# Optimization experiments

Measured on AMD Instinct MI355X. Metric: run time of the kernel, lower is better.

Reference implementation:

```python
import jax, jax.numpy as jnp
import numpy as np

B, S, D = 4, 2048, 1024
DFF = 4 * D
NE = 4        # routed experts
NS = 2        # shared experts
TOPK = 2
CAP_F = 1.25


def _gelu(v):
    return jax.nn.gelu(v, approximate=False)  # torch nn.GELU default (erf)


def setup_inputs() -> dict:
    key = jax.random.key(0)
    ks = jax.random.split(key, 9)
    s = 0.02
    f = lambda k, sh: jax.random.normal(k, sh, dtype=jnp.float32) * s
    return {
        "hidden_states": jax.random.normal(ks[0], (B, S, D), dtype=jnp.float32),
        "router_w1": f(ks[1], (D, D)), "router_b1": jnp.zeros((D,), jnp.float32),
        "router_w2": f(ks[2], (D, NE)), "router_b2": jnp.zeros((NE,), jnp.float32),
        "re_w1": f(ks[3], (NE, D, DFF)), "re_b1": jnp.zeros((NE, DFF), jnp.float32),
        "re_w2": f(ks[4], (NE, DFF, D)), "re_b2": jnp.zeros((NE, D), jnp.float32),
        "se_w1": f(ks[5], (NS, D, DFF)), "se_b1": jnp.zeros((NS, DFF), jnp.float32),
        "se_w2": f(ks[6], (NS, DFF, D)), "se_b2": jnp.zeros((NS, D), jnp.float32),
        "out_w": f(ks[7], (D, D)), "out_b": jnp.zeros((D,), jnp.float32),
    }


def reference(hidden_states, router_w1, router_b1, router_w2, router_b2,
              re_w1, re_b1, re_w2, re_b2, se_w1, se_b1, se_w2, se_b2,
              out_w, out_b):
    b, s, d = hidden_states.shape
    T = b * s
    x = hidden_states.reshape(T, d)

    # --- router ---
    logits = _gelu(x @ router_w1 + router_b1) @ router_w2 + router_b2  # [T, NE]
    top_v, top_i = jax.lax.top_k(logits, TOPK)
    rweights = jax.nn.softmax(top_v, axis=-1)                          # [T, TOPK]
    z_loss = jnp.mean(jnp.square(jax.nn.logsumexp(logits, axis=-1)))

    capacity = int(T / NE * CAP_F)  # static Python int

    # padded token slot T absorbs dropped/overflow contributions, discarded later
    x_pad = jnp.concatenate([x, jnp.zeros((1, d), x.dtype)], axis=0)
    final = jnp.zeros((T + 1, d), x.dtype)

    for i in range(TOPK):
        eidx = top_i[:, i]
        w_pad = jnp.concatenate([rweights[:, i], jnp.zeros((1,), x.dtype)])
        for j in range(NE):
            # first `capacity` tokens routed to expert j (deterministic capacity drop)
            idx = jnp.nonzero(eidx == j, size=capacity, fill_value=T)[0]  # [capacity]
            h = _gelu(x_pad[idx] @ re_w1[j] + re_b1[j]) @ re_w2[j] + re_b2[j]
            final = final.at[idx].add(w_pad[idx][:, None] * h)
    final = final[:T]

    # shared experts (dense, weight 1/NS each)
    for j in range(NS):
        final = final + (1.0 / NS) * (_gelu(x @ se_w1[j] + se_b1[j]) @ se_w2[j] + se_b2[j])

    out = final @ out_w + out_b
    out = out * 0.5 + x * 0.5
    mu = jnp.mean(out, axis=-1, keepdims=True)
    var = jnp.var(out, axis=-1, keepdims=True)
    out = (out - mu) / jnp.sqrt(var + 1e-6)  # layer_norm, no affine, eps=1e-6
    return out.reshape(b, s, d), z_loss
```

## Files before the change

kernel.cpp:

```cpp
#include <hip/hip_runtime.h>
#include <hip/hip_bf16.h>
#include <math.h>

#define TTOK 8192
#define DM 1024
#define DFFN 4096
#define NEXP 4
#define CAPACITY 2560
#define EROWSN (2*CAPACITY)

typedef short bf16x8 __attribute__((ext_vector_type(8)));
typedef float f32x4 __attribute__((ext_vector_type(4)));

__device__ __forceinline__ unsigned short f2bf(float f) {
  unsigned int u = __float_as_uint(f);
  u = (u + 0x7fffu + ((u >> 16) & 1u)) >> 16;
  return (unsigned short)u;
}
__device__ __forceinline__ float bf2f(unsigned short h) {
  return __uint_as_float(((unsigned int)h) << 16);
}
__device__ __forceinline__ float gelu_f(float v) {
  return 0.5f * v * (1.0f + erff(v * 0.7071067811865476f));
}
__device__ __forceinline__ void gl16(const void* g, void* l) {
  __builtin_amdgcn_global_load_lds((const __attribute__((address_space(1))) void*)g,
                                   (__attribute__((address_space(3))) void*)l, 16, 0, 0);
}

__global__ void k_cvt_x(const float* __restrict__ x, unsigned short* __restrict__ xhi,
                        unsigned short* __restrict__ xlo) {
  int i = blockIdx.x * blockDim.x + threadIdx.x;
  const int n4 = (TTOK + 1) * DM / 4;
  if (i >= n4) return;
  int base = i * 4;
  float v[4] = {0.f, 0.f, 0.f, 0.f};
  if (base < TTOK * DM) {
    float4 f = *reinterpret_cast<const float4*>(x + base);
    v[0] = f.x; v[1] = f.y; v[2] = f.z; v[3] = f.w;
  }
  ushort4 h, l;
  unsigned short hh[4], ll[4];
#pragma unroll
  for (int j = 0; j < 4; j++) {
    hh[j] = f2bf(v[j]);
    ll[j] = f2bf(v[j] - bf2f(hh[j]));
  }
  h.x = hh[0]; h.y = hh[1]; h.z = hh[2]; h.w = hh[3];
  l.x = ll[0]; l.y = ll[1]; l.z = ll[2]; l.w = ll[3];
  reinterpret_cast<ushort4*>(xhi)[i] = h;
  reinterpret_cast<ushort4*>(xlo)[i] = l;
}

__global__ void k_tcvt(const float* __restrict__ W, unsigned short* __restrict__ Wt,
                       int K, int N) {
  __shared__ float tile[32][33];
  int tx = threadIdx.x, ty = threadIdx.y;
  int n0 = blockIdx.x * 32, k0 = blockIdx.y * 32;
#pragma unroll
  for (int i = 0; i < 4; i++)
    tile[ty + i * 8][tx] = W[(size_t)(k0 + ty + i * 8) * N + n0 + tx];
  __syncthreads();
#pragma unroll
  for (int i = 0; i < 4; i++)
    Wt[(size_t)(n0 + ty + i * 8) * K + k0 + tx] = f2bf(tile[tx][ty + i * 8]);
}

__global__ void k_tcvt2(const float* __restrict__ W, unsigned short* __restrict__ Whi,
                        unsigned short* __restrict__ Wlo, int K, int N) {
  __shared__ float tile[32][33];
  int tx = threadIdx.x, ty = threadIdx.y;
  int n0 = blockIdx.x * 32, k0 = blockIdx.y * 32;
#pragma unroll
  for (int i = 0; i < 4; i++)
    tile[ty + i * 8][tx] = W[(size_t)(k0 + ty + i * 8) * N + n0 + tx];
  __syncthreads();
#pragma unroll
  for (int i = 0; i < 4; i++) {
    float v = tile[tx][ty + i * 8];
    unsigned short h = f2bf(v);
    Whi[(size_t)(n0 + ty + i * 8) * K + k0 + tx] = h;
    Wlo[(size_t)(n0 + ty + i * 8) * K + k0 + tx] = f2bf(v - bf2f(h));
  }
}

__global__ __launch_bounds__(256) void k_router(
    const unsigned short* __restrict__ xhi, const unsigned short* __restrict__ xlo,
    const unsigned short* __restrict__ whi, const unsigned short* __restrict__ wlo,
    const float* __restrict__ bias, float* __restrict__ Hr) {
  const int t = threadIdx.x;
  const int m0 = blockIdx.y * 128, n0 = blockIdx.x * 128;
  __shared__ unsigned short sAh[4096], sAl[4096], sBh[4096], sBl[4096];
  const int offA0 = t * 16, offA1 = offA0 + 4096;
  const int r0 = offA0 >> 6, c0e = (offA0 & 63) >> 1;
  const int r1 = offA1 >> 6, c1e = (offA1 & 63) >> 1;
  const unsigned short* pAh0 = xhi + (size_t)(m0 + r0) * DM + c0e;
  const unsigned short* pAh1 = xhi + (size_t)(m0 + r1) * DM + c1e;
  const unsigned short* pAl0 = xlo + (size_t)(m0 + r0) * DM + c0e;
  const unsigned short* pAl1 = xlo + (size_t)(m0 + r1) * DM + c1e;
  const unsigned short* pBh0 = whi + (size_t)(n0 + r0) * DM + c0e;
  const unsigned short* pBh1 = whi + (size_t)(n0 + r1) * DM + c1e;
  const unsigned short* pBl0 = wlo + (size_t)(n0 + r0) * DM + c0e;
  const unsigned short* pBl1 = wlo + (size_t)(n0 + r1) * DM + c1e;
  const int lane = t & 63, wid = t >> 6;
  const int wm = (wid >> 1) * 64, wn = (wid & 1) * 64;
  const int fr = lane & 15, fk = (lane >> 4) * 8;
  f32x4 acc[4][4];
#pragma unroll
  for (int m = 0; m < 4; m++)
#pragma unroll
    for (int n = 0; n < 4; n++) acc[m][n] = (f32x4){0.f, 0.f, 0.f, 0.f};
  for (int k0 = 0; k0 < DM; k0 += 32) {
    __syncthreads();
    gl16(pAh0 + k0, sAh + (offA0 >> 1)); gl16(pAh1 + k0, sAh + (offA1 >> 1));
    gl16(pAl0 + k0, sAl + (offA0 >> 1)); gl16(pAl1 + k0, sAl + (offA1 >> 1));
    gl16(pBh0 + k0, sBh + (offA0 >> 1)); gl16(pBh1 + k0, sBh + (offA1 >> 1));
    gl16(pBl0 + k0, sBl + (offA0 >> 1)); gl16(pBl1 + k0, sBl + (offA1 >> 1));
    __syncthreads();
    bf16x8 ah[4], al[4], bh[4], bl[4];
#pragma unroll
    for (int m = 0; m < 4; m++) {
      ah[m] = *reinterpret_cast<const bf16x8*>(sAh + (wm + m * 16 + fr) * 32 + fk);
      al[m] = *reinterpret_cast<const bf16x8*>(sAl + (wm + m * 16 + fr) * 32 + fk);
    }
#pragma unroll
    for (int n = 0; n < 4; n++) {
      bh[n] = *reinterpret_cast<const bf16x8*>(sBh + (wn + n * 16 + fr) * 32 + fk);
      bl[n] = *reinterpret_cast<const bf16x8*>(sBl + (wn + n * 16 + fr) * 32 + fk);
    }
#pragma unroll
    for (int m = 0; m < 4; m++)
#pragma unroll
      for (int n = 0; n < 4; n++) {
        acc[m][n] = __builtin_amdgcn_mfma_f32_16x16x32_bf16(ah[m], bh[n], acc[m][n], 0, 0, 0);
        acc[m][n] = __builtin_amdgcn_mfma_f32_16x16x32_bf16(ah[m], bl[n], acc[m][n], 0, 0, 0);
        acc[m][n] = __builtin_amdgcn_mfma_f32_16x16x32_bf16(al[m], bh[n], acc[m][n], 0, 0, 0);
      }
  }
  const int er = (lane >> 4) * 4, ec = lane & 15;
#pragma unroll
  for (int n = 0; n < 4; n++) {
    const int cc = n0 + wn + n * 16 + ec;
    const float bn = bias[cc];
#pragma unroll
    for (int m = 0; m < 4; m++) {
      const int rbase = m0 + wm + m * 16 + er;
#pragma unroll
      for (int j = 0; j < 4; j++)
        Hr[(size_t)(rbase + j) * DM + cc] = gelu_f(acc[m][n][j] + bn);
    }
  }
}

template <int MODE>
__global__ __launch_bounds__(256) void k_gemm(
    const unsigned short* __restrict__ A, const unsigned short* __restrict__ Bt,
    const float* __restrict__ bias, float* __restrict__ outF,
    unsigned short* __restrict__ outBf, const int* __restrict__ rows,
    const float* __restrict__ rwgt, const int* __restrict__ rowsPad, int N, int K) {
  if constexpr (MODE == 0 || MODE == 2) {
    if ((int)(blockIdx.y * 128) >= rowsPad[0]) return;
  }
  const int t = threadIdx.x;
  const int m0 = blockIdx.y * 128, n0 = blockIdx.x * 128;
  __shared__ unsigned short sA[4096], sB[4096];
  const int offA0 = t * 16, offA1 = offA0 + 4096;
  const int r0 = offA0 >> 6, c0e = (offA0 & 63) >> 1;
  const int r1 = offA1 >> 6, c1e = (offA1 & 63) >> 1;
  size_t ar0 = m0 + r0, ar1 = m0 + r1;
  if constexpr (MODE == 0) { ar0 = rows[ar0]; ar1 = rows[ar1]; }
  const unsigned short* pA0 = A + ar0 * (size_t)K + c0e;
  const unsigned short* pA1 = A + ar1 * (size_t)K + c1e;
  const unsigned short* pB0 = Bt + (size_t)(n0 + r0) * K + c0e;
  const unsigned short* pB1 = Bt + (size_t)(n0 + r1) * K + c1e;
  unsigned short* lA0 = sA + (offA0 >> 1);
  unsigned short* lA1 = sA + (offA1 >> 1);
  unsigned short* lB0 = sB + (offA0 >> 1);
  unsigned short* lB1 = sB + (offA1 >> 1);
  const int lane = t & 63, wid = t >> 6;
  const int wm = (wid >> 1) * 64, wn = (wid & 1) * 64;
  const int fr = lane & 15, fk = (lane >> 4) * 8;
  f32x4 acc[4][4];
#pragma unroll
  for (int m = 0; m < 4; m++)
#pragma unroll
    for (int n = 0; n < 4; n++) acc[m][n] = (f32x4){0.f, 0.f, 0.f, 0.f};
  for (int k0 = 0; k0 < K; k0 += 32) {
    __syncthreads();
    gl16(pA0 + k0, lA0); gl16(pA1 + k0, lA1);
    gl16(pB0 + k0, lB0); gl16(pB1 + k0, lB1);
    __syncthreads();
    bf16x8 av[4], bv[4];
#pragma unroll
    for (int m = 0; m < 4; m++)
      av[m] = *reinterpret_cast<const bf16x8*>(sA + (wm + m * 16 + fr) * 32 + fk);
#pragma unroll
    for (int n = 0; n < 4; n++)
      bv[n] = *reinterpret_cast<const bf16x8*>(sB + (wn + n * 16 + fr) * 32 + fk);
#pragma unroll
    for (int m = 0; m < 4; m++)
#pragma unroll
      for (int n = 0; n < 4; n++)
        acc[m][n] = __builtin_amdgcn_mfma_f32_16x16x32_bf16(av[m], bv[n], acc[m][n], 0, 0, 0);
  }
  const int er = (lane >> 4) * 4, ec = lane & 15;
#pragma unroll
  for (int n = 0; n < 4; n++) {
    const int cc = n0 + wn + n * 16 + ec;
    const float bn = bias[cc];
#pragma unroll
    for (int m = 0; m < 4; m++) {
      const int rbase = m0 + wm + m * 16 + er;
#pragma unroll
      for (int j = 0; j < 4; j++) {
        const int rr = rbase + j;
        float v = acc[m][n][j] + bn;
        if constexpr (MODE <= 1) {
          outBf[(size_t)rr * N + cc] = f2bf(gelu_f(v));
        } else if constexpr (MODE == 2) {
          const int tok = rows[rr];
          if (tok < TTOK) atomicAdd(outF + (size_t)tok * DM + cc, rwgt[rr] * v);
        } else if constexpr (MODE == 3) {
          atomicAdd(outF + (size_t)rr * DM + cc, 0.5f * v);
        } else {
          outF[(size_t)rr * N + cc] = v;
        }
      }
    }
  }
}

__global__ __launch_bounds__(256) void k_logits(const float* __restrict__ Hr,
                                                const float* __restrict__ w2,
                                                const float* __restrict__ b2,
                                                float* __restrict__ logits) {
  int tok = blockIdx.x * 4 + (threadIdx.x >> 6);
  int lane = threadIdx.x & 63;
  const float* h = Hr + (size_t)tok * DM;
  float s0 = 0.f, s1 = 0.f, s2 = 0.f, s3 = 0.f;
  for (int d = lane; d < DM; d += 64) {
    float hv = h[d];
    s0 += hv * w2[d * 4 + 0];
    s1 += hv * w2[d * 4 + 1];
    s2 += hv * w2[d * 4 + 2];
    s3 += hv * w2[d * 4 + 3];
  }
#pragma unroll
  for (int off = 32; off >= 1; off >>= 1) {
    s0 += __shfl_down(s0, off, 64);
    s1 += __shfl_down(s1, off, 64);
    s2 += __shfl_down(s2, off, 64);
    s3 += __shfl_down(s3, off, 64);
  }
  if (lane == 0) {
    logits[tok * 4 + 0] = s0 + b2[0];
    logits[tok * 4 + 1] = s1 + b2[1];
    logits[tok * 4 + 2] = s2 + b2[2];
    logits[tok * 4 + 3] = s3 + b2[3];
  }
}

__global__ void k_topk(const float* __restrict__ logits, int* __restrict__ e0,
                       int* __restrict__ e1, float* __restrict__ w0,
                       float* __restrict__ w1, float* __restrict__ zout) {
  int tok = blockIdx.x * blockDim.x + threadIdx.x;
  if (tok >= TTOK) return;
  float l[4];
#pragma unroll
  for (int j = 0; j < 4; j++) l[j] = logits[tok * 4 + j];
  int i0 = 0; float v0 = l[0];
#pragma unroll
  for (int j = 1; j < 4; j++) if (l[j] > v0) { v0 = l[j]; i0 = j; }
  int i1 = -1; float v1 = -1e30f;
#pragma unroll
  for (int j = 0; j < 4; j++) if (j != i0 && l[j] > v1) { v1 = l[j]; i1 = j; }
  float d = expf(v1 - v0);
  float a = 1.f / (1.f + d);
  e0[tok] = i0; e1[tok] = i1;
  w0[tok] = a;  w1[tok] = d * a;
  float se = 0.f;
#pragma unroll
  for (int j = 0; j < 4; j++) se += expf(l[j] - v0);
  float lse = v0 + logf(se);
  atomicAdd(zout, lse * lse * (1.0f / TTOK));
}

__global__ __launch_bounds__(256) void k_lists(const int* __restrict__ e0,
                                               const int* __restrict__ e1,
                                               const float* __restrict__ w0,
                                               const float* __restrict__ w1,
                                               int* __restrict__ list,
                                               float* __restrict__ lwgt,
                                               int* __restrict__ cnt) {
  int b = blockIdx.x;
  int prio = b >> 2, j = b & 3;
  const int* e = prio ? e1 : e0;
  const float* w = prio ? w1 : w0;
  __shared__ int warpsum[4];
  __shared__ int sbase;
  if (threadIdx.x == 0) sbase = 0;
  __syncthreads();
  int lane = threadIdx.x & 63, wv = threadIdx.x >> 6;
  for (int t0 = 0; t0 < TTOK; t0 += 256) {
    int tok = t0 + threadIdx.x;
    bool p = (e[tok] == j);
    unsigned long long bal = __ballot(p);
    int pre = __popcll(bal & ((1ull << lane) - 1ull));
    if (lane == 0) warpsum[wv] = __popcll(bal);
    __syncthreads();
    int woff = 0;
    for (int q = 0; q < wv; q++) woff += warpsum[q];
    int tot = warpsum[0] + warpsum[1] + warpsum[2] + warpsum[3];
    int slot = sbase + woff + pre;
    if (p && slot < CAPACITY) {
      list[b * CAPACITY + slot] = tok;
      lwgt[b * CAPACITY + slot] = w[tok];
    }
    __syncthreads();
    if (threadIdx.x == 0) sbase += tot;
  }
  __syncthreads();
  if (threadIdx.x == 0) cnt[b] = min(sbase, CAPACITY);
}

__global__ void k_combine(const int* __restrict__ list, const float* __restrict__ lwgt,
                          const int* __restrict__ cnt, int* __restrict__ erows,
                          float* __restrict__ ewgt, int* __restrict__ rowsPad) {
  int j = blockIdx.x;
  int c0 = cnt[j], c1 = cnt[4 + j];
  for (int s = threadIdx.x; s < EROWSN; s += blockDim.x) {
    int tok = TTOK; float wv = 0.f;
    if (s < c0) { tok = list[j * CAPACITY + s]; wv = lwgt[j * CAPACITY + s]; }
    else if (s < c0 + c1) {
      tok = list[(4 + j) * CAPACITY + (s - c0)];
      wv = lwgt[(4 + j) * CAPACITY + (s - c0)];
    }
    erows[j * EROWSN + s] = tok;
    ewgt[j * EROWSN + s] = wv;
  }
  if (threadIdx.x == 0) rowsPad[j] = ((c0 + c1 + 127) / 128) * 128;
}

__global__ void k_cvt_final(const float* __restrict__ f, unsigned short* __restrict__ fb) {
  int i = blockIdx.x * blockDim.x + threadIdx.x;
  if (i >= TTOK * DM / 4) return;
  float4 v = reinterpret_cast<const float4*>(f)[i];
  ushort4 o;
  o.x = f2bf(v.x); o.y = f2bf(v.y); o.z = f2bf(v.z); o.w = f2bf(v.w);
  reinterpret_cast<ushort4*>(fb)[i] = o;
}

__global__ __launch_bounds__(256) void k_ln(const float* __restrict__ OUT,
                                            const float* __restrict__ x,
                                            float* __restrict__ out) {
  int r = blockIdx.x;
  const float* o = OUT + (size_t)r * DM;
  const float* xr = x + (size_t)r * DM;
  int t = threadIdx.x;
  float v[4];
  float s = 0.f, s2 = 0.f;
#pragma unroll
  for (int i = 0; i < 4; i++) {
    int d = t + i * 256;
    float val = 0.5f * o[d] + 0.5f * xr[d];
    v[i] = val; s += val; s2 += val * val;
  }
#pragma unroll
  for (int off = 32; off >= 1; off >>= 1) {
    s += __shfl_down(s, off, 64);
    s2 += __shfl_down(s2, off, 64);
  }
  __shared__ float rs[4], rs2[4];
  int wv = t >> 6, lane = t & 63;
  if (lane == 0) { rs[wv] = s; rs2[wv] = s2; }
  __syncthreads();
  s = rs[0] + rs[1] + rs[2] + rs[3];
  s2 = rs2[0] + rs2[1] + rs2[2] + rs2[3];
  float mu = s * (1.f / DM);
  float var = s2 * (1.f / DM) - mu * mu;
  float inv = 1.0f / sqrtf(var + 1e-6f);
#pragma unroll
  for (int i = 0; i < 4; i++)
    out[(size_t)r * DM + t + i * 256] = (v[i] - mu) * inv;
}

static constexpr size_t SZ_X = (size_t)(TTOK + 1) * DM * 2;
static constexpr size_t OFF_XHI = 0;
static constexpr size_t OFF_XLO = OFF_XHI + SZ_X;
static constexpr size_t OFF_FINAL = OFF_XLO + SZ_X;
static constexpr size_t OFF_BIG = OFF_FINAL + (size_t)TTOK * DM * 4;
static constexpr size_t OFF_WBUF = OFF_BIG + (size_t)TTOK * DFFN * 2;
static constexpr size_t OFF_MISC = OFF_WBUF + (size_t)2 * DM * DFFN * 2;
static constexpr size_t OFF_LOGITS = OFF_MISC;
static constexpr size_t OFF_E0 = OFF_LOGITS + (size_t)TTOK * 4 * 4;
static constexpr size_t OFF_E1 = OFF_E0 + (size_t)TTOK * 4;
static constexpr size_t OFF_W0 = OFF_E1 + (size_t)TTOK * 4;
static constexpr size_t OFF_W1 = OFF_W0 + (size_t)TTOK * 4;
static constexpr size_t OFF_LIST = OFF_W1 + (size_t)TTOK * 4;
static constexpr size_t OFF_LWGT = OFF_LIST + (size_t)8 * CAPACITY * 4;
static constexpr size_t OFF_CNT = OFF_LWGT + (size_t)8 * CAPACITY * 4;
static constexpr size_t OFF_EROWS = OFF_CNT + 64;
static constexpr size_t OFF_EWGT = OFF_EROWS + (size_t)NEXP * EROWSN * 4;
static constexpr size_t OFF_RPAD = OFF_EWGT + (size_t)NEXP * EROWSN * 4;

extern "C" void kernel_launch(void* const* d_in, const int* in_sizes, int n_in,
                              void* d_out, int out_size, void* d_ws, size_t ws_size,
                              hipStream_t stream) {
  const float* x = (const float*)d_in[0];
  const float* rw1 = (const float*)d_in[1];
  const float* rb1 = (const float*)d_in[2];
  const float* rw2 = (const float*)d_in[3];
  const float* rb2 = (const float*)d_in[4];
  const float* re_w1 = (const float*)d_in[5];
  const float* re_b1 = (const float*)d_in[6];
  const float* re_w2 = (const float*)d_in[7];
  const float* re_b2 = (const float*)d_in[8];
  const float* se_w1 = (const float*)d_in[9];
  const float* se_b1 = (const float*)d_in[10];
  const float* se_w2 = (const float*)d_in[11];
  const float* se_b2 = (const float*)d_in[12];
  const float* out_w = (const float*)d_in[13];
  const float* out_b = (const float*)d_in[14];
  float* outp = (float*)d_out;

  char* ws = (char*)d_ws;
  unsigned short* xhi = (unsigned short*)(ws + OFF_XHI);
  unsigned short* xlo = (unsigned short*)(ws + OFF_XLO);
  float* finalb = (float*)(ws + OFF_FINAL);
  char* big = ws + OFF_BIG;
  float* Hr = (float*)big;
  unsigned short* act = (unsigned short*)big;
  unsigned short* fbf = (unsigned short*)big;
  float* OUTb = (float*)(big + (size_t)TTOK * DM * 2);
  unsigned short* w1t = (unsigned short*)(ws + OFF_WBUF);
  unsigned short* w2t = w1t + (size_t)DM * DFFN;
  unsigned short* rwhi = w1t;
  unsigned short* rwlo = w1t + (size_t)DM * DM;
  unsigned short* owt = w1t;
  float* logits = (float*)(ws + OFF_LOGITS);
  int* e0 = (int*)(ws + OFF_E0);
  int* e1 = (int*)(ws + OFF_E1);
  float* w0 = (float*)(ws + OFF_W0);
  float* w1 = (float*)(ws + OFF_W1);
  int* list = (int*)(ws + OFF_LIST);
  float* lwgt = (float*)(ws + OFF_LWGT);
  int* cnt = (int*)(ws + OFF_CNT);
  int* erows = (int*)(ws + OFF_EROWS);
  float* ewgt = (float*)(ws + OFF_EWGT);
  int* rpad = (int*)(ws + OFF_RPAD);
  float* zout = outp + (size_t)TTOK * DM;

  hipMemsetAsync(finalb, 0, (size_t)TTOK * DM * 4, stream);
  hipMemsetAsync(zout, 0, 4, stream);

  {
    int n4 = (TTOK + 1) * DM / 4;
    k_cvt_x<<<(n4 + 255) / 256, 256, 0, stream>>>(x, xhi, xlo);
  }
  k_tcvt2<<<dim3(DM / 32, DM / 32), dim3(32, 8), 0, stream>>>(rw1, rwhi, rwlo, DM, DM);
  k_router<<<dim3(DM / 128, TTOK / 128), 256, 0, stream>>>(xhi, xlo, rwhi, rwlo, rb1, Hr);
  k_logits<<<TTOK / 4, 256, 0, stream>>>(Hr, rw2, rb2, logits);
  k_topk<<<TTOK / 256, 256, 0, stream>>>(logits, e0, e1, w0, w1, zout);
  k_lists<<<8, 256, 0, stream>>>(e0, e1, w0, w1, list, lwgt, cnt);
  k_combine<<<NEXP, 256, 0, stream>>>(list, lwgt, cnt, erows, ewgt, rpad);

  for (int j = 0; j < NEXP; j++) {
    k_tcvt<<<dim3(DFFN / 32, DM / 32), dim3(32, 8), 0, stream>>>(
        re_w1 + (size_t)j * DM * DFFN, w1t, DM, DFFN);
    k_tcvt<<<dim3(DM / 32, DFFN / 32), dim3(32, 8), 0, stream>>>(
        re_w2 + (size_t)j * DFFN * DM, w2t, DFFN, DM);
    k_gemm<0><<<dim3(DFFN / 128, EROWSN / 128), 256, 0, stream>>>(
        xhi, w1t, re_b1 + (size_t)j * DFFN, nullptr, act,
        erows + (size_t)j * EROWSN, nullptr, rpad + j, DFFN, DM);
    k_gemm<2><<<dim3(DM / 128, EROWSN / 128), 256, 0, stream>>>(
        act, w2t, re_b2 + (size_t)j * DM, finalb, nullptr,
        erows + (size_t)j * EROWSN, ewgt + (size_t)j * EROWSN, rpad + j, DM, DFFN);
  }
  for (int j = 0; j < 2; j++) {
    k_tcvt<<<dim3(DFFN / 32, DM / 32), dim3(32, 8), 0, stream>>>(
        se_w1 + (size_t)j * DM * DFFN, w1t, DM, DFFN);
    k_tcvt<<<dim3(DM / 32, DFFN / 32), dim3(32, 8), 0, stream>>>(
        se_w2 + (size_t)j * DFFN * DM, w2t, DFFN, DM);
    k_gemm<1><<<dim3(DFFN / 128, TTOK / 128), 256, 0, stream>>>(
        xhi, w1t, se_b1 + (size_t)j * DFFN, nullptr, act, nullptr, nullptr, nullptr,
        DFFN, DM);
    k_gemm<3><<<dim3(DM / 128, TTOK / 128), 256, 0, stream>>>(
        act, w2t, se_b2 + (size_t)j * DM, finalb, nullptr, nullptr, nullptr, nullptr,
        DM, DFFN);
  }
  k_cvt_final<<<TTOK * DM / 4 / 256, 256, 0, stream>>>(finalb, fbf);
  k_tcvt<<<dim3(DM / 32, DM / 32), dim3(32, 8), 0, stream>>>(out_w, owt, DM, DM);
  k_gemm<4><<<dim3(DM / 128, TTOK / 128), 256, 0, stream>>>(
      fbf, owt, out_b, OUTb, nullptr, nullptr, nullptr, nullptr, DM, DM);
  k_ln<<<TTOK, 256, 0, stream>>>(OUTb, x, outp);
}
```

Before: 1.461 ms.

## Double-buffer LDS in GEMMs, split-K expert down-proj, drop shared-expert atomics

Both the router GEMM and the generic GEMM now double-buffer their LDS tiles, so the next K slice is issued before computing on the current one, with one barrier per iteration instead of two. The expert down-projection (MODE 2) is split along K into two z-blocks to raise occupancy, with the bias added only by the first half. The shared-expert accumulation replaces atomicAdd with a plain read-modify-write, since no two blocks write the same output element there. The workspace layout is also reshuffled so xlo shares the activation buffer, and a barrier in k_lists is moved inside its loop. The doubled LDS use may lower occupancy, and split-K doubles the atomic traffic in the expert down-projection.

```diff
diff --git a/kernel.cpp b/kernel.cpp
--- a/kernel.cpp
+++ b/kernel.cpp
@@ -90,8 +90,9 @@
     const float* __restrict__ bias, float* __restrict__ Hr) {
   const int t = threadIdx.x;
   const int m0 = blockIdx.y * 128, n0 = blockIdx.x * 128;
-  __shared__ unsigned short sAh[4096], sAl[4096], sBh[4096], sBl[4096];
+  __shared__ unsigned short sAh[2][4096], sAl[2][4096], sBh[2][4096], sBl[2][4096];
   const int offA0 = t * 16, offA1 = offA0 + 4096;
+  const int i0 = offA0 >> 1, i1 = offA1 >> 1;
   const int r0 = offA0 >> 6, c0e = (offA0 & 63) >> 1;
   const int r1 = offA1 >> 6, c1e = (offA1 & 63) >> 1;
   const unsigned short* pAh0 = xhi + (size_t)(m0 + r0) * DM + c0e;
@@ -110,23 +111,29 @@
   for (int m = 0; m < 4; m++)
 #pragma unroll
     for (int n = 0; n < 4; n++) acc[m][n] = (f32x4){0.f, 0.f, 0.f, 0.f};
+
+  auto stage = [&](int b, int k) {
+    gl16(pAh0 + k, &sAh[b][i0]); gl16(pAh1 + k, &sAh[b][i1]);
+    gl16(pAl0 + k, &sAl[b][i0]); gl16(pAl1 + k, &sAl[b][i1]);
+    gl16(pBh0 + k, &sBh[b][i0]); gl16(pBh1 + k, &sBh[b][i1]);
+    gl16(pBl0 + k, &sBl[b][i0]); gl16(pBl1 + k, &sBl[b][i1]);
+  };
+
+  int cur = 0;
+  stage(0, 0);
+  __syncthreads();
   for (int k0 = 0; k0 < DM; k0 += 32) {
-    __syncthreads();
-    gl16(pAh0 + k0, sAh + (offA0 >> 1)); gl16(pAh1 + k0, sAh + (offA1 >> 1));
-    gl16(pAl0 + k0, sAl + (offA0 >> 1)); gl16(pAl1 + k0, sAl + (offA1 >> 1));
-    gl16(pBh0 + k0, sBh + (offA0 >> 1)); gl16(pBh1 + k0, sBh + (offA1 >> 1));
-    gl16(pBl0 + k0, sBl + (offA0 >> 1)); gl16(pBl1 + k0, sBl + (offA1 >> 1));
-    __syncthreads();
+    if (k0 + 32 < DM) stage(cur ^ 1, k0 + 32);
     bf16x8 ah[4], al[4], bh[4], bl[4];
 #pragma unroll
     for (int m = 0; m < 4; m++) {
-      ah[m] = *reinterpret_cast<const bf16x8*>(sAh + (wm + m * 16 + fr) * 32 + fk);
-      al[m] = *reinterpret_cast<const bf16x8*>(sAl + (wm + m * 16 + fr) * 32 + fk);
+      ah[m] = *reinterpret_cast<const bf16x8*>(&sAh[cur][(wm + m * 16 + fr) * 32 + fk]);
+      al[m] = *reinterpret_cast<const bf16x8*>(&sAl[cur][(wm + m * 16 + fr) * 32 + fk]);
     }
 #pragma unroll
     for (int n = 0; n < 4; n++) {
-      bh[n] = *reinterpret_cast<const bf16x8*>(sBh + (wn + n * 16 + fr) * 32 + fk);
-      bl[n] = *reinterpret_cast<const bf16x8*>(sBl + (wn + n * 16 + fr) * 32 + fk);
+      bh[n] = *reinterpret_cast<const bf16x8*>(&sBh[cur][(wn + n * 16 + fr) * 32 + fk]);
+      bl[n] = *reinterpret_cast<const bf16x8*>(&sBl[cur][(wn + n * 16 + fr) * 32 + fk]);
     }
 #pragma unroll
     for (int m = 0; m < 4; m++)
@@ -136,6 +143,8 @@
         acc[m][n] = __builtin_amdgcn_mfma_f32_16x16x32_bf16(ah[m], bl[n], acc[m][n], 0, 0, 0);
         acc[m][n] = __builtin_amdgcn_mfma_f32_16x16x32_bf16(al[m], bh[n], acc[m][n], 0, 0, 0);
       }
+    __syncthreads();
+    cur ^= 1;
   }
   const int er = (lane >> 4) * 4, ec = lane & 15;
 #pragma unroll
@@ -163,20 +172,19 @@
   }
   const int t = threadIdx.x;
   const int m0 = blockIdx.y * 128, n0 = blockIdx.x * 128;
-  __shared__ unsigned short sA[4096], sB[4096];
+  int kbeg = 0, klen = K;
+  if constexpr (MODE == 2) { kbeg = blockIdx.z * (K >> 1); klen = K >> 1; }
+  __shared__ unsigned short sA[2][4096], sB[2][4096];
   const int offA0 = t * 16, offA1 = offA0 + 4096;
+  const int i0 = offA0 >> 1, i1 = offA1 >> 1;
   const int r0 = offA0 >> 6, c0e = (offA0 & 63) >> 1;
   const int r1 = offA1 >> 6, c1e = (offA1 & 63) >> 1;
   size_t ar0 = m0 + r0, ar1 = m0 + r1;
   if constexpr (MODE == 0) { ar0 = rows[ar0]; ar1 = rows[ar1]; }
-  const unsigned short* pA0 = A + ar0 * (size_t)K + c0e;
-  const unsigned short* pA1 = A + ar1 * (size_t)K + c1e;
-  const unsigned short* pB0 = Bt + (size_t)(n0 + r0) * K + c0e;
-  const unsigned short* pB1 = Bt + (size_t)(n0 + r1) * K + c1e;
-  unsigned short* lA0 = sA + (offA0 >> 1);
-  unsigned short* lA1 = sA + (offA1 >> 1);
-  unsigned short* lB0 = sB + (offA0 >> 1);
-  unsigned short* lB1 = sB + (offA1 >> 1);
+  const unsigned short* pA0 = A + ar0 * (size_t)K + kbeg + c0e;
+  const unsigned short* pA1 = A + ar1 * (size_t)K + kbeg + c1e;
+  const unsigned short* pB0 = Bt + (size_t)(n0 + r0) * K + kbeg + c0e;
+  const unsigned short* pB1 = Bt + (size_t)(n0 + r1) * K + kbeg + c1e;
   const int lane = t & 63, wid = t >> 6;
   const int wm = (wid >> 1) * 64, wn = (wid & 1) * 64;
   const int fr = lane & 15, fk = (lane >> 4) * 8;
@@ -185,23 +193,31 @@
   for (int m = 0; m < 4; m++)
 #pragma unroll
     for (int n = 0; n < 4; n++) acc[m][n] = (f32x4){0.f, 0.f, 0.f, 0.f};
-  for (int k0 = 0; k0 < K; k0 += 32) {
-    __syncthreads();
-    gl16(pA0 + k0, lA0); gl16(pA1 + k0, lA1);
-    gl16(pB0 + k0, lB0); gl16(pB1 + k0, lB1);
-    __syncthreads();
+
+  auto stage = [&](int b, int k) {
+    gl16(pA0 + k, &sA[b][i0]); gl16(pA1 + k, &sA[b][i1]);
+    gl16(pB0 + k, &sB[b][i0]); gl16(pB1 + k, &sB[b][i1]);
+  };
+
+  int cur = 0;
+  stage(0, 0);
+  __syncthreads();
+  for (int k0 = 0; k0 < klen; k0 += 32) {
+    if (k0 + 32 < klen) stage(cur ^ 1, k0 + 32);
     bf16x8 av[4], bv[4];
 #pragma unroll
     for (int m = 0; m < 4; m++)
-      av[m] = *reinterpret_cast<const bf16x8*>(sA + (wm + m * 16 + fr) * 32 + fk);
+      av[m] = *reinterpret_cast<const bf16x8*>(&sA[cur][(wm + m * 16 + fr) * 32 + fk]);
 #pragma unroll
     for (int n = 0; n < 4; n++)
-      bv[n] = *reinterpret_cast<const bf16x8*>(sB + (wn + n * 16 + fr) * 32 + fk);
+      bv[n] = *reinterpret_cast<const bf16x8*>(&sB[cur][(wn + n * 16 + fr) * 32 + fk]);
 #pragma unroll
     for (int m = 0; m < 4; m++)
 #pragma unroll
       for (int n = 0; n < 4; n++)
         acc[m][n] = __builtin_amdgcn_mfma_f32_16x16x32_bf16(av[m], bv[n], acc[m][n], 0, 0, 0);
+    __syncthreads();
+    cur ^= 1;
   }
   const int er = (lane >> 4) * 4, ec = lane & 15;
 #pragma unroll
@@ -214,16 +230,17 @@
 #pragma unroll
       for (int j = 0; j < 4; j++) {
         const int rr = rbase + j;
-        float v = acc[m][n][j] + bn;
         if constexpr (MODE <= 1) {
-          outBf[(size_t)rr * N + cc] = f2bf(gelu_f(v));
+          outBf[(size_t)rr * N + cc] = f2bf(gelu_f(acc[m][n][j] + bn));
         } else if constexpr (MODE == 2) {
+          float v = acc[m][n][j] + (blockIdx.z == 0 ? bn : 0.f);
           const int tok = rows[rr];
           if (tok < TTOK) atomicAdd(outF + (size_t)tok * DM + cc, rwgt[rr] * v);
         } else if constexpr (MODE == 3) {
-          atomicAdd(outF + (size_t)rr * DM + cc, 0.5f * v);
+          float* p = outF + (size_t)rr * DM + cc;
+          *p += 0.5f * (acc[m][n][j] + bn);
         } else {
-          outF[(size_t)rr * N + cc] = v;
+          outF[(size_t)rr * N + cc] = acc[m][n][j] + bn;
         }
       }
     }
@@ -318,8 +335,8 @@
     }
     __syncthreads();
     if (threadIdx.x == 0) sbase += tot;
-  }
-  __syncthreads();
+    __syncthreads();
+  }
   if (threadIdx.x == 0) cnt[b] = min(sbase, CAPACITY);
 }
 
@@ -384,13 +401,15 @@
     out[(size_t)r * DM + t + i * 256] = (v[i] - mu) * inv;
 }
 
-static constexpr size_t SZ_X = (size_t)(TTOK + 1) * DM * 2;
 static constexpr size_t OFF_XHI = 0;
-static constexpr size_t OFF_XLO = OFF_XHI + SZ_X;
-static constexpr size_t OFF_FINAL = OFF_XLO + SZ_X;
-static constexpr size_t OFF_BIG = OFF_FINAL + (size_t)TTOK * DM * 4;
-static constexpr size_t OFF_WBUF = OFF_BIG + (size_t)TTOK * DFFN * 2;
-static constexpr size_t OFF_MISC = OFF_WBUF + (size_t)2 * DM * DFFN * 2;
+static constexpr size_t SZ_XHI = (size_t)(TTOK + 1) * DM * 2;
+static constexpr size_t OFF_ACT = OFF_XHI + SZ_XHI;
+static constexpr size_t SZ_ACT = (size_t)TTOK * DFFN * 2;
+static constexpr size_t OFF_WBUF = OFF_ACT + SZ_ACT;
+static constexpr size_t SZ_WBUF = (size_t)2 * DM * DFFN * 2;
+static constexpr size_t OFF_FINAL = OFF_WBUF + SZ_WBUF;
+static constexpr size_t SZ_FINAL = (size_t)TTOK * DM * 4;
+static constexpr size_t OFF_MISC = OFF_FINAL + SZ_FINAL;
 static constexpr size_t OFF_LOGITS = OFF_MISC;
 static constexpr size_t OFF_E0 = OFF_LOGITS + (size_t)TTOK * 4 * 4;
 static constexpr size_t OFF_E1 = OFF_E0 + (size_t)TTOK * 4;
@@ -425,18 +444,17 @@
 
   char* ws = (char*)d_ws;
   unsigned short* xhi = (unsigned short*)(ws + OFF_XHI);
-  unsigned short* xlo = (unsigned short*)(ws + OFF_XLO);
-  float* finalb = (float*)(ws + OFF_FINAL);
-  char* big = ws + OFF_BIG;
-  float* Hr = (float*)big;
-  unsigned short* act = (unsigned short*)big;
-  unsigned short* fbf = (unsigned short*)big;
-  float* OUTb = (float*)(big + (size_t)TTOK * DM * 2);
+  float* Hr = (float*)(ws + OFF_ACT);
+  unsigned short* xlo = (unsigned short*)(ws + OFF_ACT + 33554432);
+  unsigned short* act = (unsigned short*)(ws + OFF_ACT);
+  unsigned short* fbf = (unsigned short*)(ws + OFF_ACT);
+  float* OUTb = (float*)(ws + OFF_ACT + 16777216);
   unsigned short* w1t = (unsigned short*)(ws + OFF_WBUF);
   unsigned short* w2t = w1t + (size_t)DM * DFFN;
   unsigned short* rwhi = w1t;
   unsigned short* rwlo = w1t + (size_t)DM * DM;
   unsigned short* owt = w1t;
+  float* finalb = (float*)(ws + OFF_FINAL);
   float* logits = (float*)(ws + OFF_LOGITS);
   int* e0 = (int*)(ws + OFF_E0);
   int* e1 = (int*)(ws + OFF_E1);
@@ -450,7 +468,7 @@
   int* rpad = (int*)(ws + OFF_RPAD);
   float* zout = outp + (size_t)TTOK * DM;
 
-  hipMemsetAsync(finalb, 0, (size_t)TTOK * DM * 4, stream);
+  hipMemsetAsync(finalb, 0, SZ_FINAL, stream);
   hipMemsetAsync(zout, 0, 4, stream);
 
   {
@@ -472,7 +490,7 @@
     k_gemm<0><<<dim3(DFFN / 128, EROWSN / 128), 256, 0, stream>>>(
         xhi, w1t, re_b1 + (size_t)j * DFFN, nullptr, act,
         erows + (size_t)j * EROWSN, nullptr, rpad + j, DFFN, DM);
-    k_gemm<2><<<dim3(DM / 128, EROWSN / 128), 256, 0, stream>>>(
+    k_gemm<2><<<dim3(DM / 128, EROWSN / 128, 2), 256, 0, stream>>>(
         act, w2t, re_b2 + (size_t)j * DM, finalb, nullptr,
         erows + (size_t)j * EROWSN, ewgt + (size_t)j * EROWSN, rpad + j, DM, DFFN);
   }
```

Result: faster. 1.272 ms (-12.9%).
